# Optimization experiments

Measured on AMD Instinct MI355X. Metric: run time of the kernel, lower is better.

The kernel has to match this reference:

```python
import jax, jax.numpy as jnp
import numpy as np


def lrelu(x):
    return jax.nn.leaky_relu(x, 0.1)


def mask_softmax(a, mask, axis=-1):
    # faithful to the torch version: max over ALL entries, mask applied post-exp
    a_max = jnp.max(a, axis=axis, keepdims=True)
    e = jnp.exp(a - a_max) * mask
    return e / (jnp.sum(e, axis=axis, keepdims=True) + 1e-6)


def gru_cell(x, h, w_ih, w_hh, b_ih, b_hh):
    # torch.nn.GRUCell math; weights stored as [in, 3H]
    gi = x @ w_ih + b_ih
    gh = h @ w_hh + b_hh
    ir, iz, inn = jnp.split(gi, 3, axis=-1)
    hr, hz, hn = jnp.split(gh, 3, axis=-1)
    r = jax.nn.sigmoid(ir + hr)
    z = jax.nn.sigmoid(iz + hz)
    n = jnp.tanh(inn + r * hn)
    return (1 - z) * n + z * h


def setup_inputs() -> dict:
    key = jax.random.key(0)
    B, N, M, E, H, D, K = 128, 256, 12, 256, 128, 3, 2
    AF, BF, NA, NB = 82, 6, 100, 12
    ks = iter(jax.random.split(key, 64))
    nrm = lambda shape: jax.random.normal(next(ks), shape, jnp.float32) * 0.05
    return dict(
        batch_size=B,
        vertex_mask=jnp.ones((B, N), jnp.float32),
        vertex=jax.random.randint(next(ks), (B, N), 0, NA, dtype=jnp.int32),
        edge=jax.random.randint(next(ks), (B, E), 0, NB, dtype=jnp.int32),
        atom_adj=jax.random.randint(next(ks), (B * N * M,), 0, B * N, dtype=jnp.int32),
        bond_adj=jax.random.randint(next(ks), (B * N * M,), 0, B * E, dtype=jnp.int32),
        nbs_mask=jnp.ones((B, N, M), jnp.float32),
        init_atom_features=nrm((NA, AF)),
        init_bond_features=nrm((NB, BF)),
        emb_w=nrm((AF, H)), emb_b=nrm((H,)),
        Wa_main_w=nrm((D, K, H, H)), Wa_main_b=nrm((D, K, H)),
        Wbmm_w=nrm((D, K, H)), Wbmm_b=nrm((D, K)),
        Wmain_w=nrm((D, K, H, H)), Wmain_b=nrm((D, K, H)),
        Wm2s_w=nrm((D, K * H, H)), Wm2s_b=nrm((D, H)),
        Ws2m_w=nrm((D, H, H)), Ws2m_b=nrm((D, H)),
        Wsuper_w=nrm((D, H, H)), Wsuper_b=nrm((D, H)),
        Wzm1_w=nrm((D, H, H)), Wzm1_b=nrm((D, H)),
        Wzm2_w=nrm((D, H, H)), Wzm2_b=nrm((D, H)),
        Wzs1_w=nrm((D, H, H)), Wzs1_b=nrm((D, H)),
        Wzs2_w=nrm((D, H, H)), Wzs2_b=nrm((D, H)),
        U2_w=nrm((D, H + BF, H)), U2_b=nrm((D, H)),
        U1_w=nrm((D, 2 * H, H)), U1_b=nrm((D, H)),
        gm_wih=nrm((H, 3 * H)), gm_whh=nrm((H, 3 * H)), gm_bih=nrm((3 * H,)), gm_bhh=nrm((3 * H,)),
        gs_wih=nrm((H, 3 * H)), gs_whh=nrm((H, 3 * H)), gs_bih=nrm((3 * H,)), gs_bhh=nrm((3 * H,)),
    )


def reference(batch_size, vertex_mask, vertex, edge, atom_adj, bond_adj, nbs_mask,
              init_atom_features, init_bond_features, emb_w, emb_b,
              Wa_main_w, Wa_main_b, Wbmm_w, Wbmm_b, Wmain_w, Wmain_b,
              Wm2s_w, Wm2s_b, Ws2m_w, Ws2m_b, Wsuper_w, Wsuper_b,
              Wzm1_w, Wzm1_b, Wzm2_w, Wzm2_b, Wzs1_w, Wzs1_b, Wzs2_w, Wzs2_b,
              U2_w, U2_b, U1_w, U1_b,
              gm_wih, gm_whh, gm_bih, gm_bhh, gs_wih, gs_whh, gs_bih, gs_bhh):
    B = batch_size
    N = vertex_mask.shape[1]
    M = nbs_mask.shape[2]
    H = emb_w.shape[1]
    BF = init_bond_features.shape[1]
    D, K = Wa_main_w.shape[0], Wa_main_w.shape[1]

    vertex_initial = init_atom_features[vertex]          # [B,N,AF]
    edge_initial = init_bond_features[edge]              # [B,E,BF]
    vf = lrelu(vertex_initial @ emb_w + emb_b)           # [B,N,H]
    vm = vertex_mask[:, :, None]
    sf = jnp.sum(vf * vm, axis=1, keepdims=True)         # [B,1,H] super node

    for d in range(D):
        # multi-head super-node attention (all k heads vectorized)
        a_main = jnp.tanh(jnp.einsum('bnh,khg->bkng', vf, Wa_main_w[d]) + Wa_main_b[d][None, :, None, :])
        a = jnp.einsum('bkng,kg->bkn', a_main * sf[:, None, :, :], Wbmm_w[d]) + Wbmm_b[d][None, :, None]
        attn = mask_softmax(a, vertex_mask[:, None, :])                  # [B,K,N]
        wv = jnp.einsum('bnh,khg->bkng', vf, Wmain_w[d]) + Wmain_b[d][None, :, None, :]
        m = jnp.einsum('bkn,bkng->bkg', attn, wv).reshape(B, 1, K * H)   # head-concat
        main_to_super = jnp.tanh(m @ Wm2s_w[d] + Wm2s_b[d])              # [B,1,H]

        # WLN unit: gather neighbor atom/bond features, fused MLP + masked sum
        vnei = vf.reshape(-1, H)[atom_adj].reshape(B, N, M, H)
        enei = edge_initial.reshape(-1, BF)[bond_adj].reshape(B, N, M, BF)
        nei = jnp.concatenate([vnei, enei], axis=-1)                     # [B,N,M,H+BF]
        nei_label = lrelu(nei @ U2_w[d] + U2_b[d])
        nei_label = jnp.sum(nei_label * nbs_mask[..., None], axis=-2)    # [B,N,H]
        main_self = lrelu(jnp.concatenate([vf, nei_label], axis=-1) @ U1_w[d] + U1_b[d])

        super_to_main = jnp.tanh(sf @ Ws2m_w[d] + Ws2m_b[d])
        super_self = jnp.tanh(sf @ Wsuper_w[d] + Wsuper_b[d])

        z_main = jax.nn.sigmoid(main_self @ Wzm1_w[d] + Wzm1_b[d]
                                + super_to_main @ Wzm2_w[d] + Wzm2_b[d])
        hidden_main = (1 - z_main) * main_self + z_main * super_to_main
        vf = gru_cell(hidden_main.reshape(-1, H), vf.reshape(-1, H),
                      gm_wih, gm_whh, gm_bih, gm_bhh).reshape(B, N, H)

        z_super = jax.nn.sigmoid(super_self @ Wzs1_w[d] + Wzs1_b[d]
                                 + main_to_super @ Wzs2_w[d] + Wzs2_b[d])
        hidden_super = (1 - z_super) * super_self + z_super * main_to_super
        sf = gru_cell(hidden_super.reshape(B, H), sf.reshape(B, H),
                      gs_wih, gs_whh, gs_bih, gs_bhh).reshape(B, 1, H)

    return (vf, sf)
```

## Files before the change

### kernel.cpp

```cpp
#include <hip/hip_runtime.h>

typedef unsigned short ushort_t;
typedef unsigned int uint_t;
typedef unsigned char uchar_t;
typedef __attribute__((ext_vector_type(8))) short short8;
typedef __attribute__((ext_vector_type(4))) float f32x4;
typedef __attribute__((ext_vector_type(2))) float f32x2;

#define B   128
#define Nv  256
#define Mn  12
#define Hd  128
#define Dd  3
#define Kk  2
#define AFd 82
#define BFd 6
#define BN  (B*Nv)

enum { EPI_NONE = 0, EPI_LRELU = 1 };

__device__ __forceinline__ float lrelu(float x) { return fmaxf(x, 0.1f * x); }
__device__ __forceinline__ float sigmoidf(float x) { return 1.f / (1.f + expf(-x)); }
__device__ __forceinline__ ushort_t f2b(float x) {
    uint_t u = __float_as_uint(x);
// ... 230 lines not shown
            for (int nf = 0; nf < 4; ++nf) {
                const int c = wn * 64 + nf * 16 + lr;
                #pragma unroll
                for (int reg = 0; reg < 4; ++reg) {
                    const int r = wm * 32 + mf * 16 + lg * 4 + reg;
                    Pout[(size_t)(row0 + r) * Hd + c] = f2e8(acc[mf][nf][reg] + u2B[c]);
                }
            }
    } else {
        #pragma unroll
        for (int mf = 0; mf < 2; ++mf) {
            #pragma unroll
            for (int reg = 0; reg < 4; ++reg) {
                float p = 0.f;
                #pragma unroll
                for (int nf = 0; nf < 4; ++nf) {
                    const int c = wn * 64 + nf * 16 + lr;
                    p += tanhf(acc[mf][nf][reg] + EBb[c]) * EUs[c];
                }
                p += __shfl_xor(p, 1); p += __shfl_xor(p, 2);
                p += __shfl_xor(p, 4); p += __shfl_xor(p, 8);
                if (lr == 0) red[wm * 32 + mf * 16 + lg * 4 + reg][wn] = p;
            }
        }
        __syncthreads();
        if (t < 64) {
            const int gr = row0 + t;
            a_out[(size_t)(gr >> 8) * 512 + (size_t)ky * 256 + (gr & 255)] =
                red[t][0] + red[t][1] + wbmmB[ky];
        }
    }
}

__global__ __launch_bounds__(256, 3) void k_mega(
    const ushort_t* __restrict__ vfb,
    const uchar_t* __restrict__ P8,
    const ushort_t* __restrict__ qt,
    const int* __restrict__ aadj, const int* __restrict__ badj,
    const int* __restrict__ edge, const float* __restrict__ nmask,
    const ushort_t* __restrict__ wt_u1,
    const ushort_t* __restrict__ wt_zm1,
    const ushort_t* __restrict__ wt_rz,
    const ushort_t* __restrict__ wt_inn,
    const ushort_t* __restrict__ wt_hn,
    const float* __restrict__ u1b,
    const float* __restrict__ zm1b,
    const float* __restrict__ bih, const float* __restrict__ bhh,
    const float* __restrict__ czm2, const float* __restrict__ s2m,
    void* __restrict__ outv, const int finalFp32)
{
    const int t = threadIdx.x;
    const int lane = t & 63, w = t >> 6;
    const int wm = w >> 1, wn = w & 1;
    const int lr = lane & 15, lg = lane >> 4;
    const int row0 = blockIdx.x * 64;
    const int b = row0 >> 8;

    __shared__ ushort_t As[64 * 256];
    __shared__ ushort_t aiS[64 * Mn];
    __shared__ ushort_t eiS[64 * Mn];
    __shared__ ushort_t mkS[64 * Mn];

    for (int i = t; i < 64 * Mn; i += 256) {
        const int r = i / Mn, m = i - r * Mn;
        const long g = (long)(row0 + r) * Mn + m;
        aiS[i] = (ushort_t)aadj[g];
        eiS[i] = (ushort_t)edge[badj[g]];
        mkS[i] = f2b(nmask[g]);
    }
    {
        const int r_st = t >> 2, q4 = t & 3;
        const ushort_t* src = vfb + (size_t)(row0 + r_st) * Hd + q4 * 32;
        #pragma unroll
        for (int j = 0; j < 4; ++j) {
            uint4 v = ((const uint4*)src)[j];
            int byte = r_st * 512 + q4 * 64 + j * 16;
            byte ^= ((r_st & 7) << 4);
            *(uint4*)((char*)As + byte) = v;
        }
    }
    __syncthreads();

    #pragma unroll 1
    for (int it = 0; it < 4; ++it) {
        const int idx = it * 256 + t;
        const int r = idx >> 4, h0 = (idx & 15) * 8;
        float a8[8] = {0.f,0.f,0.f,0.f,0.f,0.f,0.f,0.f};
        #pragma unroll
        for (int m = 0; m < Mn; ++m) {
            const int ai = aiS[r * Mn + m];
            const float mk = b2f(mkS[r * Mn + m]);
            const uint2 pv = *(const uint2*)&P8[(size_t)ai * Hd + h0];
            const uint4 qv = *(const uint4*)&qt[(size_t)eiS[r * Mn + m] * Hd + h0];
            const f32x2 p01 = __builtin_amdgcn_cvt_pk_f32_fp8((int)pv.x, false);
            const f32x2 p23 = __builtin_amdgcn_cvt_pk_f32_fp8((int)pv.x, true);
            const f32x2 p45 = __builtin_amdgcn_cvt_pk_f32_fp8((int)pv.y, false);
            const f32x2 p67 = __builtin_amdgcn_cvt_pk_f32_fp8((int)pv.y, true);
            const float pf[8] = {p01[0], p01[1], p23[0], p23[1], p45[0], p45[1], p67[0], p67[1]};
            const ushort_t* qq = (const ushort_t*)&qv;
            #pragma unroll
            for (int e = 0; e < 8; ++e) {
                const float v = pf[e] + b2f(qq[e]);
                a8[e] = fmaf(mk, lrelu(v), a8[e]);
            }
        }
        ushort_t o8[8];
        #pragma unroll
        for (int e = 0; e < 8; ++e) o8[e] = f2b(a8[e]);
        int byte = r * 512 + (128 + h0) * 2;
        byte ^= ((r & 7) << 4);
        *(uint4*)((char*)As + byte) = *(const uint4*)o8;
    }
    __syncthreads();

    f32x4 acc[2][4];

#define ZERO_ACC() { _Pragma("unroll") for (int i = 0; i < 2; ++i) _Pragma("unroll") for (int j = 0; j < 4; ++j) acc[i][j] = (f32x4){0.f,0.f,0.f,0.f}; }
#define GEMM_PASS(WG, KPADW, KTOT, AOFF_EXPR) { \
        ZERO_ACC(); \
        _Pragma("unroll") \
        for (int kk = 0; kk < (KTOT); kk += 32) { \
            const int acol = (AOFF_EXPR); \
            short8 af[2], bfr[4]; \
            _Pragma("unroll") \
            for (int nf = 0; nf < 4; ++nf) { \
                const int col = wn * 64 + nf * 16 + lr; \
                bfr[nf] = *(const short8*)((WG) + (size_t)col * (KPADW) + kk + lg * 8); \
            } \
            _Pragma("unroll") \
            for (int mf = 0; mf < 2; ++mf) { \
                const int row = wm * 32 + mf * 16 + lr; \
                int byte = row * 512 + (acol + lg * 8) * 2; \
                byte ^= ((row & 7) << 4); \
                af[mf] = *(const short8*)((const char*)As + byte); \
            } \
            _Pragma("unroll") \
            for (int mf = 0; mf < 2; ++mf) \
                _Pragma("unroll") \
                for (int nf = 0; nf < 4; ++nf) \
                    acc[mf][nf] = __builtin_amdgcn_mfma_f32_16x16x32_bf16(af[mf], bfr[nf], acc[mf][nf], 0, 0, 0); \
        } }

    GEMM_PASS(wt_u1, 256, 256, kk);
    {
// ... 91 lines not shown
            const float r2 = sigmoidf(acc[mf][nf][2] + bb);
            const float r3 = sigmoidf(acc[mf][nf][3] + bb);
            const float n0 = tanhf(upk_lo(innp[mf][nf][0]) + r0 * upk_lo(hnp[mf][nf][0]));
            const float n1 = tanhf(upk_hi(innp[mf][nf][0]) + r1 * upk_hi(hnp[mf][nf][0]));
            const float n2 = tanhf(upk_lo(innp[mf][nf][1]) + r2 * upk_lo(hnp[mf][nf][1]));
            const float n3 = tanhf(upk_hi(innp[mf][nf][1]) + r3 * upk_hi(hnp[mf][nf][1]));
            innp[mf][nf][0] = pk2(n0, n1);
            innp[mf][nf][1] = pk2(n2, n3);
        }
    GEMM_PASS(wt_rz + 128 * 256, 256, 256, (kk < 128) ? (128 + kk) : (kk - 128));
    #pragma unroll
    for (int mf = 0; mf < 2; ++mf)
        #pragma unroll
        for (int nf = 0; nf < 4; ++nf) {
            const int c = wn * 64 + nf * 16 + lr;
            const float bb = bih[128 + c] + bhh[128 + c];
            #pragma unroll
            for (int reg = 0; reg < 4; ++reg) {
                const int rl = wm * 32 + mf * 16 + lg * 4 + reg;
                const float z = sigmoidf(acc[mf][nf][reg] + bb);
                const uint_t np = innp[mf][nf][reg >> 1];
                const float n = (reg & 1) ? upk_hi(np) : upk_lo(np);
                int byte = rl * 512 + c * 2;
                byte ^= ((rl & 7) << 4);
                const float h = b2f(*(const ushort_t*)((const char*)As + byte));
                const float o = (1.f - z) * n + z * h;
                const size_t oidx = (size_t)(row0 + rl) * Hd + c;
                if (finalFp32) ((float*)outv)[oidx] = o;
                else           ((ushort_t*)outv)[oidx] = f2b(o);
            }
        }
#undef GEMM_PASS
#undef ZERO_ACC
}

__device__ __forceinline__ void gemv1(const float* __restrict__ W0, const float* __restrict__ x0,
                                      int ldw, int off, int K,
                                      float (*red)[8][32][4],
                                      float* __restrict__ y0, int t)
{
    const int gq = t & 31, hs = t >> 5;
    const int hn = K >> 3;
    f32x4 a0 = (f32x4){0.f,0.f,0.f,0.f};
    const float* Wp0 = W0 + off + (size_t)gq * 4;
    const int h0 = hs * hn;
    #pragma unroll 8
    for (int i = 0; i < hn; ++i) {
        const float4 w0 = *(const float4*)&Wp0[(size_t)(h0 + i) * ldw];
        const float v0 = x0[h0 + i];
        a0.x = fmaf(v0, w0.x, a0.x); a0.y = fmaf(v0, w0.y, a0.y);
        a0.z = fmaf(v0, w0.z, a0.z); a0.w = fmaf(v0, w0.w, a0.w);
    }
    *(f32x4*)&red[0][hs][gq][0] = a0;
    __syncthreads();
    if (t < 128) {
        float s0 = 0.f;
        #pragma unroll
        for (int p = 0; p < 8; ++p) s0 += red[0][p][t >> 2][t & 3];
        y0[t] = s0;
    }
    __syncthreads();
}

__device__ __forceinline__ void gemv2(const float* __restrict__ W0, const float* __restrict__ x0,
                                      const float* __restrict__ W1, const float* __restrict__ x1,
                                      int ldw, int off, int K,
                                      float (*red)[8][32][4],
                                      float* __restrict__ y0, float* __restrict__ y1, int t)
{
    const int gq = t & 31, hs = t >> 5;
    const int hn = K >> 3;
    f32x4 a0 = (f32x4){0.f,0.f,0.f,0.f}, a1 = (f32x4){0.f,0.f,0.f,0.f};
    const float* Wp0 = W0 + off + (size_t)gq * 4;
    const float* Wp1 = W1 + off + (size_t)gq * 4;
    const int h0 = hs * hn;
    #pragma unroll 4
    for (int i = 0; i < hn; ++i) {
        const float4 w0 = *(const float4*)&Wp0[(size_t)(h0 + i) * ldw];
        const float4 w1 = *(const float4*)&Wp1[(size_t)(h0 + i) * ldw];
        const float v0 = x0[h0 + i], v1 = x1[h0 + i];
        a0.x = fmaf(v0, w0.x, a0.x); a0.y = fmaf(v0, w0.y, a0.y);
        a0.z = fmaf(v0, w0.z, a0.z); a0.w = fmaf(v0, w0.w, a0.w);
        a1.x = fmaf(v1, w1.x, a1.x); a1.y = fmaf(v1, w1.y, a1.y);
        a1.z = fmaf(v1, w1.z, a1.z); a1.w = fmaf(v1, w1.w, a1.w);
    }
    *(f32x4*)&red[0][hs][gq][0] = a0;
    *(f32x4*)&red[1][hs][gq][0] = a1;
    __syncthreads();
    if (t < 128) {
        float s0 = 0.f, s1 = 0.f;
        #pragma unroll
        for (int p = 0; p < 8; ++p) {
            s0 += red[0][p][t >> 2][t & 3];
            s1 += red[1][p][t >> 2][t & 3];
        }
        y0[t] = s0; y1[t] = s1;
    }
    __syncthreads();
}

__device__ __forceinline__ void gemv3(const float* __restrict__ W0, const float* __restrict__ x0,
                                      const float* __restrict__ W1, const float* __restrict__ x1,
                                      const float* __restrict__ W2, const float* __restrict__ x2,
                                      int ldw, int off, int K,
                                      float (*red)[8][32][4],
                                      float* __restrict__ y0, float* __restrict__ y1,
                                      float* __restrict__ y2, int t)
{
    const int gq = t & 31, hs = t >> 5;
    const int hn = K >> 3;
    f32x4 a0 = (f32x4){0.f,0.f,0.f,0.f}, a1 = (f32x4){0.f,0.f,0.f,0.f}, a2 = (f32x4){0.f,0.f,0.f,0.f};
    const float* Wp0 = W0 + off + (size_t)gq * 4;
    const float* Wp1 = W1 + off + (size_t)gq * 4;
    const float* Wp2 = W2 + off + (size_t)gq * 4;
    const int h0 = hs * hn;
    #pragma unroll 4
    for (int i = 0; i < hn; ++i) {
        const float4 w0 = *(const float4*)&Wp0[(size_t)(h0 + i) * ldw];
        const float4 w1 = *(const float4*)&Wp1[(size_t)(h0 + i) * ldw];
        const float4 w2 = *(const float4*)&Wp2[(size_t)(h0 + i) * ldw];
        const float v0 = x0[h0 + i], v1 = x1[h0 + i], v2 = x2[h0 + i];
        a0.x = fmaf(v0, w0.x, a0.x); a0.y = fmaf(v0, w0.y, a0.y);
        a0.z = fmaf(v0, w0.z, a0.z); a0.w = fmaf(v0, w0.w, a0.w);
        a1.x = fmaf(v1, w1.x, a1.x); a1.y = fmaf(v1, w1.y, a1.y);
        a1.z = fmaf(v1, w1.z, a1.z); a1.w = fmaf(v1, w1.w, a1.w);
        a2.x = fmaf(v2, w2.x, a2.x); a2.y = fmaf(v2, w2.y, a2.y);
        a2.z = fmaf(v2, w2.z, a2.z); a2.w = fmaf(v2, w2.w, a2.w);
    }
    *(f32x4*)&red[0][hs][gq][0] = a0;
    *(f32x4*)&red[1][hs][gq][0] = a1;
    *(f32x4*)&red[2][hs][gq][0] = a2;
    __syncthreads();
    if (t < 128) {
        float s0 = 0.f, s1 = 0.f, s2 = 0.f;
        #pragma unroll
        for (int p = 0; p < 8; ++p) {
            s0 += red[0][p][t >> 2][t & 3];
            s1 += red[1][p][t >> 2][t & 3];
            s2 += red[2][p][t >> 2][t & 3];
        }
        y0[t] = s0; y1[t] = s1; y2[t] = s2;
    }
    __syncthreads();
}

__global__ __launch_bounds__(256) void k_super(
    const float* __restrict__ a_buf, const float* __restrict__ vmask,
    const ushort_t* __restrict__ vfb,
    const float* __restrict__ sf_in,
    const float* __restrict__ Wm, const float* __restrict__ bm,
    const float* __restrict__ Wm2s, const float* __restrict__ bm2s,
    const float* __restrict__ Ws2m, const float* __restrict__ bs2m,
    const float* __restrict__ Wsup, const float* __restrict__ bsup,
    const float* __restrict__ Wzm2, const float* __restrict__ bzm2,
    const float* __restrict__ Wzs1, const float* __restrict__ bzs1,
    const float* __restrict__ Wzs2, const float* __restrict__ bzs2,
    const float* __restrict__ gwih, const float* __restrict__ gwhh,
    const float* __restrict__ gbih, const float* __restrict__ gbhh,
    float* __restrict__ s2m_g, float* __restrict__ czm2_g,
    float* __restrict__ sf_out)
{
    const int b = blockIdx.x, t = threadIdx.x;
    const int wid = t >> 6, lane = t & 63;
    __shared__ float red[3][8][32][4];
    __shared__ float att0[256], att1[256];
    __shared__ float sfl[128], tbA[128], tbB[128], mv[256];
    __shared__ float ms2[128], s2ml[128], ssl[128], hsl[128];
    __shared__ float tmp1[128], tmp2[128], tmp3[128];
    __shared__ float gib[384], ghb[384];
    __shared__ float saS[2];
    __shared__ float lm[4][2], ls[4][2];

    const float v0 = a_buf[(size_t)b * 512 + t];
    const float v1 = a_buf[(size_t)b * 512 + 256 + t];
    const float vm = vmask[b * Nv + t];
    float m0 = v0, m1 = v1;
    #pragma unroll
    for (int o = 1; o < 64; o <<= 1) {
        m0 = fmaxf(m0, __shfl_xor(m0, o));
        m1 = fmaxf(m1, __shfl_xor(m1, o));
    }
    if (lane == 0) { lm[wid][0] = m0; lm[wid][1] = m1; }
    __syncthreads();
    m0 = fmaxf(fmaxf(lm[0][0], lm[1][0]), fmaxf(lm[2][0], lm[3][0]));
    m1 = fmaxf(fmaxf(lm[0][1], lm[1][1]), fmaxf(lm[2][1], lm[3][1]));
    const float e0v = expf(v0 - m0) * vm;
    const float e1v = expf(v1 - m1) * vm;
    float s0 = e0v, s1 = e1v;
    #pragma unroll
    for (int o = 1; o < 64; o <<= 1) {
        s0 += __shfl_xor(s0, o);
        s1 += __shfl_xor(s1, o);
    }
    if (lane == 0) { ls[wid][0] = s0; ls[wid][1] = s1; }
    if (t < 128) sfl[t] = sf_in[b * Hd + t];
    __syncthreads();
    s0 = ls[0][0] + ls[1][0] + ls[2][0] + ls[3][0];
    s1 = ls[0][1] + ls[1][1] + ls[2][1] + ls[3][1];
    att0[t] = e0v / (s0 + 1e-6f);
    att1[t] = e1v / (s1 + 1e-6f);
    if (t == 0) { saS[0] = s0 / (s0 + 1e-6f); saS[1] = s1 / (s1 + 1e-6f); }
    __syncthreads();

    {
        const int hq = t & 31, ns = t >> 5;
        f32x4 a0 = (f32x4){0.f,0.f,0.f,0.f}, a1 = (f32x4){0.f,0.f,0.f,0.f};
        const ushort_t* base = vfb + (size_t)b * Nv * Hd + hq * 4;
        #pragma unroll 8
        for (int i = 0; i < 32; ++i) {
            const int n = ns * 32 + i;
            float xv[4];
            b2f4(*(const uint2*)&base[(size_t)n * Hd], xv);
            const float w0 = att0[n], w1 = att1[n];
            a0.x = fmaf(w0, xv[0], a0.x); a0.y = fmaf(w0, xv[1], a0.y);
            a0.z = fmaf(w0, xv[2], a0.z); a0.w = fmaf(w0, xv[3], a0.w);
            a1.x = fmaf(w1, xv[0], a1.x); a1.y = fmaf(w1, xv[1], a1.y);
            a1.z = fmaf(w1, xv[2], a1.z); a1.w = fmaf(w1, xv[3], a1.w);
        }
        *(f32x4*)&red[0][ns][hq][0] = a0;
        *(f32x4*)&red[1][ns][hq][0] = a1;
        __syncthreads();
        if (t < 128) {
            float u0 = 0.f, u1 = 0.f;
            #pragma unroll
            for (int p = 0; p < 8; ++p) {
                u0 += red[0][p][t >> 2][t & 3];
                u1 += red[1][p][t >> 2][t & 3];
            }
            tbA[t] = u0; tbB[t] = u1;
        }
        __syncthreads();
    }

    gemv2(Wm, tbA, Wm + Hd * Hd, tbB, Hd, 0, Hd, red, mv, mv + 128, t);
    mv[t] += saS[t >> 7] * bm[t];
    __syncthreads();

    gemv1(Wm2s, mv, Hd, 0, 2 * Hd, red, tmp1, t);
    if (t < 128) ms2[t] = tanhf(tmp1[t] + bm2s[t]);
    __syncthreads();

    gemv2(Ws2m, sfl, Wsup, sfl, Hd, 0, Hd, red, tmp1, tmp2, t);
    if (t < 128) {
        const float v = tanhf(tmp1[t] + bs2m[t]);
        s2ml[t] = v; s2m_g[b * Hd + t] = v;
        ssl[t] = tanhf(tmp2[t] + bsup[t]);
    }
    __syncthreads();

    gemv3(Wzm2, s2ml, Wzs1, ssl, Wzs2, ms2, Hd, 0, Hd, red, tmp1, tmp2, tmp3, t);
    if (t < 128) {
        czm2_g[b * Hd + t] = tmp1[t] + bzm2[t];
        const float zs = sigmoidf(tmp2[t] + bzs1[t] + tmp3[t] + bzs2[t]);
        hsl[t] = (1.f - zs) * ssl[t] + zs * ms2[t];
    }
    __syncthreads();

    #pragma unroll 1
    for (int c = 0; c < 3; ++c)
        gemv2(gwih, hsl, gwhh, sfl, 3 * Hd, c * Hd, Hd, red, gib + c * Hd, ghb + c * Hd, t);
    if (t < 128) {
        const float r = sigmoidf(gib[t] + gbih[t] + ghb[t] + gbhh[t]);
        const float z = sigmoidf(gib[128 + t] + gbih[128 + t] + ghb[128 + t] + gbhh[128 + t]);
        const float n = tanhf(gib[256 + t] + gbih[256 + t] + r * (ghb[256 + t] + gbhh[256 + t]));
        sf_out[b * Hd + t] = (1.f - z) * n + z * sfl[t];
    }
}

__global__ __launch_bounds__(256) void k_sfv(const ushort_t* __restrict__ vfb,
                                             const float* __restrict__ vmask,
                                             float* __restrict__ sf)
{
    const int b = blockIdx.x, t = threadIdx.x;
    __shared__ float vm[256];
    __shared__ float red[8][32][4];
    vm[t] = vmask[b * Nv + t];
    __syncthreads();
    const int hq = t & 31, ns = t >> 5;
    f32x4 acc = (f32x4){0.f,0.f,0.f,0.f};
    const ushort_t* base = vfb + (size_t)b * Nv * Hd + hq * 4;
    #pragma unroll 8
    for (int i = 0; i < 32; ++i) {
        const int n = ns * 32 + i;
        float xv[4];
        b2f4(*(const uint2*)&base[(size_t)n * Hd], xv);
        const float w = vm[n];
        acc.x = fmaf(w, xv[0], acc.x); acc.y = fmaf(w, xv[1], acc.y);
        acc.z = fmaf(w, xv[2], acc.z); acc.w = fmaf(w, xv[3], acc.w);
    }
    *(f32x4*)&red[ns][hq][0] = acc;
    __syncthreads();
    if (t < 128) {
        float s = 0.f;
        #pragma unroll
        for (int p = 0; p < 8; ++p) s += red[p][t >> 2][t & 3];
        sf[b * Hd + t] = s;
    }
}

// ... 23 lines not shown
    const float* Wm2s_b = (const float*)d_in[18];
    const float* Ws2m_w = (const float*)d_in[19];
    const float* Ws2m_b = (const float*)d_in[20];
    const float* Wsup_w = (const float*)d_in[21];
    const float* Wsup_b = (const float*)d_in[22];
    const float* Wzm1_w = (const float*)d_in[23];
    const float* Wzm1_b = (const float*)d_in[24];
    const float* Wzm2_w = (const float*)d_in[25];
    const float* Wzm2_b = (const float*)d_in[26];
    const float* Wzs1_w = (const float*)d_in[27];
    const float* Wzs1_b = (const float*)d_in[28];
    const float* Wzs2_w = (const float*)d_in[29];
    const float* Wzs2_b = (const float*)d_in[30];
    const float* U2_w   = (const float*)d_in[31];
    const float* U2_b   = (const float*)d_in[32];
    const float* U1_w   = (const float*)d_in[33];
    const float* U1_b   = (const float*)d_in[34];
    const float* gm_wih = (const float*)d_in[35];
    const float* gm_whh = (const float*)d_in[36];
    const float* gm_bih = (const float*)d_in[37];
    const float* gm_bhh = (const float*)d_in[38];
    const float* gs_wih = (const float*)d_in[39];
    const float* gs_whh = (const float*)d_in[40];
    const float* gs_bih = (const float*)d_in[41];
    const float* gs_bhh = (const float*)d_in[42];

    const size_t MB = 1u << 20;
    if (ws_size < 40 * MB) return;

    char* base = (char*)d_ws;
    ushort_t* VF0 = (ushort_t*)base;
    ushort_t* VF1 = (ushort_t*)(base + 8 * MB);
    uchar_t*  P8  = (uchar_t*)(base + 16 * MB);
    ushort_t* WT  = (ushort_t*)(base + 24 * MB);
    ushort_t* QT  = (ushort_t*)(base + 26 * MB);
    float*    S   = (float*)(base + 27 * MB);

    float* sfA    = S;
    float* sfB    = S + 16384;
    float* a_buf  = S + 32768;
    float* s2m    = S + 98304;
    float* c_zm2  = S + 114688;

    float* X1 = (float*)d_out;
    float* sf_final = X1 + (size_t)BN * Hd;

    const int OFF_EMB = 0;
    const int PERD = 98304;
    const int OFF_L0 = 16384;
    const int OFF_RZ = OFF_L0 + 3 * PERD;
    const int OFF_NH = OFF_RZ + 65536;

    PrepJobs PJ;
    int nj = 0, blk0 = 0;
    auto addJob = [&](const float* W, int K, int ldw, long sStride, int nPer,
                      int Kspan, int KpadRow, int kDst, int ncols, int outOff) {
        PrepJob& J = PJ.j[nj++];
        J.W = W; J.K = K; J.ldw = ldw; J.sliceStride = sStride; J.nPerSlice = nPer;
        J.Kspan = Kspan; J.KpadRow = KpadRow; J.kDst = kDst;
        J.total = ncols * Kspan; J.outOff = outOff; J.blockStart = blk0;
        blk0 += (J.total + 255) / 256;
    };
    addJob(emb_w, AFd, Hd, 0, Hd, 128, 128, 0, 128, OFF_EMB);
    for (int d = 0; d < Dd; ++d) {
        const int o = OFF_L0 + d * PERD;
        addJob(Wa_w + (long)d * Kk * Hd * Hd, Hd, Hd, (long)Hd * Hd, Hd, 128, 128, 0, 256, o);
        addJob(U2_w + (long)d * (Hd + BFd) * Hd, Hd, Hd, 0, Hd, 128, 128, 0, 128, o + 32768);
        addJob(U1_w + (long)d * 2 * Hd * Hd, 2 * Hd, Hd, 0, Hd, 256, 256, 0, 128, o + 49152);
        addJob(Wzm1_w + (long)d * Hd * Hd, Hd, Hd, 0, Hd, 128, 128, 0, 128, o + 81920);
    }
    addJob(gm_wih, Hd, 3 * Hd, 0, 256, 128, 256, 0,   256, OFF_RZ);
    addJob(gm_whh, Hd, 3 * Hd, 0, 256, 128, 256, 128, 256, OFF_RZ);
    addJob(gm_wih + 256, Hd, 3 * Hd, 0, 128, 128, 128, 0, 128, OFF_NH);
    addJob(gm_whh + 256, Hd, 3 * Hd, 0, 128, 128, 128, 0, 128, OFF_NH + 16384);
    PJ.nJobs = nj;
    k_prep_all<<<dim3(blk0), dim3(256), 0, stream>>>(PJ, WT);
    k_qtab<<<dim3(Dd), dim3(256), 0, stream>>>(init_bond, U2_w, QT);

    const dim3 blk(256);
    const dim3 g1(BN / 64, 1);

    mgemm<EPI_LRELU, false, true><<<g1, blk, 0, stream>>>(
        init_atom, AFd, AFd, vertex,
        WT + OFF_EMB, 128, emb_b, VF0, Hd);
    k_sfv<<<dim3(B), blk, 0, stream>>>(VF0, vertex_mask, sfA);

    for (int d = 0; d < Dd; ++d) {
        ushort_t* vin  = (d & 1) ? VF1 : VF0;
        ushort_t* vout = (d & 1) ? VF0 : VF1;
        float* sin  = (d & 1) ? sfB : sfA;
        float* sout = (d == Dd - 1) ? sf_final : ((d & 1) ? sfA : sfB);

        const int o = OFF_L0 + d * PERD;

        k_tdp<<<dim3(BN / 64, 3), blk, 0, stream>>>(
            vin, WT + o,
            Wa_b + (long)d * Kk * Hd, U2_b + (long)d * Hd,
            sin, Wbmm_w + (long)d * Kk * Hd, Wbmm_b + (long)d * Kk,
            a_buf, P8);

        k_super<<<dim3(B), blk, 0, stream>>>(
            a_buf, vertex_mask, vin, sin,
            Wm_w + (long)d * Kk * Hd * Hd, Wm_b + (long)d * Kk * Hd,
            Wm2s_w + (long)d * Kk * Hd * Hd, Wm2s_b + (long)d * Hd,
            Ws2m_w + (long)d * Hd * Hd, Ws2m_b + (long)d * Hd,
            Wsup_w + (long)d * Hd * Hd, Wsup_b + (long)d * Hd,
            Wzm2_w + (long)d * Hd * Hd, Wzm2_b + (long)d * Hd,
            Wzs1_w + (long)d * Hd * Hd, Wzs1_b + (long)d * Hd,
            Wzs2_w + (long)d * Hd * Hd, Wzs2_b + (long)d * Hd,
            gs_wih, gs_whh, gs_bih, gs_bhh,
            s2m, c_zm2, sout);

        k_mega<<<g1, blk, 0, stream>>>(
            vin, P8, QT + (size_t)d * 12 * Hd,
            atom_adj, bond_adj, edge, nbs_mask,
            WT + o + 49152, WT + o + 81920,
            WT + OFF_RZ, WT + OFF_NH, WT + OFF_NH + 16384,
            U1_b + (long)d * Hd, Wzm1_b + (long)d * Hd,
            gm_bih, gm_bhh,
            c_zm2, s2m,
            (d == Dd - 1) ? (void*)X1 : (void*)vout, (d == Dd - 1) ? 1 : 0);
    }
}
```

Measured before the change: 343.4 us.

## Move neighbor gather into super-node kernel to overlap with serial GEMV work

The per-atom neighbor gather-and-reduce (fp8 P plus bond Q, leaky-relu, masked sum) moves out of k_mega into extra blocks of the super-node kernel, which writes the result to a new NEI workspace buffer. k_super ran only 128 blocks of serial GEMVs, so the gather blocks can fill the idle CUs alongside them, and k_mega now just loads the precomputed NEI rows into shared memory. The cost is an extra global write and read of a 64K×128 bf16 buffer, plus a larger combined launch whose blocks differ in shared-memory footprint.

```diff
diff --git a/kernel.cpp b/kernel.cpp
--- a/kernel.cpp
+++ b/kernel.cpp
@@ -286,12 +286,292 @@
     }
 }
 
+__device__ __forceinline__ void gemv1(const float* __restrict__ W0, const float* __restrict__ x0,
+                                      int ldw, int off, int K,
+                                      float (*red)[8][32][4],
+                                      float* __restrict__ y0, int t)
+{
+    const int gq = t & 31, hs = t >> 5;
+    const int hn = K >> 3;
+    f32x4 a0 = (f32x4){0.f,0.f,0.f,0.f};
+    const float* Wp0 = W0 + off + (size_t)gq * 4;
+    const int h0 = hs * hn;
+    #pragma unroll 8
+    for (int i = 0; i < hn; ++i) {
+        const float4 w0 = *(const float4*)&Wp0[(size_t)(h0 + i) * ldw];
+        const float v0 = x0[h0 + i];
+        a0.x = fmaf(v0, w0.x, a0.x); a0.y = fmaf(v0, w0.y, a0.y);
+        a0.z = fmaf(v0, w0.z, a0.z); a0.w = fmaf(v0, w0.w, a0.w);
+    }
+    *(f32x4*)&red[0][hs][gq][0] = a0;
+    __syncthreads();
+    if (t < 128) {
+        float s0 = 0.f;
+        #pragma unroll
+        for (int p = 0; p < 8; ++p) s0 += red[0][p][t >> 2][t & 3];
+        y0[t] = s0;
+    }
+    __syncthreads();
+}
+
+__device__ __forceinline__ void gemv2(const float* __restrict__ W0, const float* __restrict__ x0,
+                                      const float* __restrict__ W1, const float* __restrict__ x1,
+                                      int ldw, int off, int K,
+                                      float (*red)[8][32][4],
+                                      float* __restrict__ y0, float* __restrict__ y1, int t)
+{
+    const int gq = t & 31, hs = t >> 5;
+    const int hn = K >> 3;
+    f32x4 a0 = (f32x4){0.f,0.f,0.f,0.f}, a1 = (f32x4){0.f,0.f,0.f,0.f};
+    const float* Wp0 = W0 + off + (size_t)gq * 4;
+    const float* Wp1 = W1 + off + (size_t)gq * 4;
+    const int h0 = hs * hn;
+    #pragma unroll 4
+    for (int i = 0; i < hn; ++i) {
+        const float4 w0 = *(const float4*)&Wp0[(size_t)(h0 + i) * ldw];
+        const float4 w1 = *(const float4*)&Wp1[(size_t)(h0 + i) * ldw];
+        const float v0 = x0[h0 + i], v1 = x1[h0 + i];
+        a0.x = fmaf(v0, w0.x, a0.x); a0.y = fmaf(v0, w0.y, a0.y);
+        a0.z = fmaf(v0, w0.z, a0.z); a0.w = fmaf(v0, w0.w, a0.w);
+        a1.x = fmaf(v1, w1.x, a1.x); a1.y = fmaf(v1, w1.y, a1.y);
+        a1.z = fmaf(v1, w1.z, a1.z); a1.w = fmaf(v1, w1.w, a1.w);
+    }
+    *(f32x4*)&red[0][hs][gq][0] = a0;
+    *(f32x4*)&red[1][hs][gq][0] = a1;
+    __syncthreads();
+    if (t < 128) {
+        float s0 = 0.f, s1 = 0.f;
+        #pragma unroll
+        for (int p = 0; p < 8; ++p) {
+            s0 += red[0][p][t >> 2][t & 3];
+            s1 += red[1][p][t >> 2][t & 3];
+        }
+        y0[t] = s0; y1[t] = s1;
+    }
+    __syncthreads();
+}
+
+__device__ __forceinline__ void gemv3(const float* __restrict__ W0, const float* __restrict__ x0,
+                                      const float* __restrict__ W1, const float* __restrict__ x1,
+                                      const float* __restrict__ W2, const float* __restrict__ x2,
+                                      int ldw, int off, int K,
+                                      float (*red)[8][32][4],
+                                      float* __restrict__ y0, float* __restrict__ y1,
+                                      float* __restrict__ y2, int t)
+{
+    const int gq = t & 31, hs = t >> 5;
+    const int hn = K >> 3;
+    f32x4 a0 = (f32x4){0.f,0.f,0.f,0.f}, a1 = (f32x4){0.f,0.f,0.f,0.f}, a2 = (f32x4){0.f,0.f,0.f,0.f};
+    const float* Wp0 = W0 + off + (size_t)gq * 4;
+    const float* Wp1 = W1 + off + (size_t)gq * 4;
+    const float* Wp2 = W2 + off + (size_t)gq * 4;
+    const int h0 = hs * hn;
+    #pragma unroll 4
+    for (int i = 0; i < hn; ++i) {
+        const float4 w0 = *(const float4*)&Wp0[(size_t)(h0 + i) * ldw];
+        const float4 w1 = *(const float4*)&Wp1[(size_t)(h0 + i) * ldw];
+        const float4 w2 = *(const float4*)&Wp2[(size_t)(h0 + i) * ldw];
+        const float v0 = x0[h0 + i], v1 = x1[h0 + i], v2 = x2[h0 + i];
+        a0.x = fmaf(v0, w0.x, a0.x); a0.y = fmaf(v0, w0.y, a0.y);
+        a0.z = fmaf(v0, w0.z, a0.z); a0.w = fmaf(v0, w0.w, a0.w);
+        a1.x = fmaf(v1, w1.x, a1.x); a1.y = fmaf(v1, w1.y, a1.y);
+        a1.z = fmaf(v1, w1.z, a1.z); a1.w = fmaf(v1, w1.w, a1.w);
+        a2.x = fmaf(v2, w2.x, a2.x); a2.y = fmaf(v2, w2.y, a2.y);
+        a2.z = fmaf(v2, w2.z, a2.z); a2.w = fmaf(v2, w2.w, a2.w);
+    }
+    *(f32x4*)&red[0][hs][gq][0] = a0;
+    *(f32x4*)&red[1][hs][gq][0] = a1;
+    *(f32x4*)&red[2][hs][gq][0] = a2;
+    __syncthreads();
+    if (t < 128) {
+        float s0 = 0.f, s1 = 0.f, s2 = 0.f;
+        #pragma unroll
+        for (int p = 0; p < 8; ++p) {
+            s0 += red[0][p][t >> 2][t & 3];
+            s1 += red[1][p][t >> 2][t & 3];
+            s2 += red[2][p][t >> 2][t & 3];
+        }
+        y0[t] = s0; y1[t] = s1; y2[t] = s2;
+    }
+    __syncthreads();
+}
+
+__global__ __launch_bounds__(256) void k_gsup(
+    const float* __restrict__ a_buf, const float* __restrict__ vmask,
+    const ushort_t* __restrict__ vfb,
+    const float* __restrict__ sf_in,
+    const float* __restrict__ Wm, const float* __restrict__ bm,
+    const float* __restrict__ Wm2s, const float* __restrict__ bm2s,
+    const float* __restrict__ Ws2m, const float* __restrict__ bs2m,
+    const float* __restrict__ Wsup, const float* __restrict__ bsup,
+    const float* __restrict__ Wzm2, const float* __restrict__ bzm2,
+    const float* __restrict__ Wzs1, const float* __restrict__ bzs1,
+    const float* __restrict__ Wzs2, const float* __restrict__ bzs2,
+    const float* __restrict__ gwih, const float* __restrict__ gwhh,
+    const float* __restrict__ gbih, const float* __restrict__ gbhh,
+    float* __restrict__ s2m_g, float* __restrict__ czm2_g,
+    float* __restrict__ sf_out,
+    const uchar_t* __restrict__ P8, const ushort_t* __restrict__ qt,
+    const int* __restrict__ aadj, const int* __restrict__ badj,
+    const int* __restrict__ edge, const float* __restrict__ nmask,
+    ushort_t* __restrict__ nei)
+{
+    const int t = threadIdx.x;
+
+    if (blockIdx.x >= B) {
+        __shared__ ushort_t aiS[64 * Mn];
+        __shared__ ushort_t eiS[64 * Mn];
+        __shared__ ushort_t mkS[64 * Mn];
+        const int row0 = (blockIdx.x - B) * 64;
+        for (int i = t; i < 64 * Mn; i += 256) {
+            const int r = i / Mn, m = i - r * Mn;
+            const long g = (long)(row0 + r) * Mn + m;
+            aiS[i] = (ushort_t)aadj[g];
+            eiS[i] = (ushort_t)edge[badj[g]];
+            mkS[i] = f2b(nmask[g]);
+        }
+        __syncthreads();
+        #pragma unroll 1
+        for (int it = 0; it < 4; ++it) {
+            const int idx = it * 256 + t;
+            const int r = idx >> 4, h0 = (idx & 15) * 8;
+            float a8[8] = {0.f,0.f,0.f,0.f,0.f,0.f,0.f,0.f};
+            #pragma unroll
+            for (int m = 0; m < Mn; ++m) {
+                const int ai = aiS[r * Mn + m];
+                const float mk = b2f(mkS[r * Mn + m]);
+                const uint2 pv = *(const uint2*)&P8[(size_t)ai * Hd + h0];
+                const uint4 qv = *(const uint4*)&qt[(size_t)eiS[r * Mn + m] * Hd + h0];
+                const f32x2 p01 = __builtin_amdgcn_cvt_pk_f32_fp8((int)pv.x, false);
+                const f32x2 p23 = __builtin_amdgcn_cvt_pk_f32_fp8((int)pv.x, true);
+                const f32x2 p45 = __builtin_amdgcn_cvt_pk_f32_fp8((int)pv.y, false);
+                const f32x2 p67 = __builtin_amdgcn_cvt_pk_f32_fp8((int)pv.y, true);
+                const float pf[8] = {p01[0], p01[1], p23[0], p23[1], p45[0], p45[1], p67[0], p67[1]};
+                const ushort_t* qq = (const ushort_t*)&qv;
+                #pragma unroll
+                for (int e = 0; e < 8; ++e) {
+                    const float v = pf[e] + b2f(qq[e]);
+                    a8[e] = fmaf(mk, lrelu(v), a8[e]);
+                }
+            }
+            ushort_t o8[8];
+            #pragma unroll
+            for (int e = 0; e < 8; ++e) o8[e] = f2b(a8[e]);
+            *(uint4*)&nei[(size_t)(row0 + r) * Hd + h0] = *(const uint4*)o8;
+        }
+        return;
+    }
+
+    const int b = blockIdx.x;
+    const int wid = t >> 6, lane = t & 63;
+    __shared__ float red[3][8][32][4];
+    __shared__ float att0[256], att1[256];
+    __shared__ float sfl[128], tbA[128], tbB[128], mv[256];
+    __shared__ float ms2[128], s2ml[128], ssl[128], hsl[128];
+    __shared__ float tmp1[128], tmp2[128], tmp3[128];
+    __shared__ float gib[384], ghb[384];
+    __shared__ float saS[2];
+    __shared__ float lm[4][2], ls[4][2];
+
+    const float v0 = a_buf[(size_t)b * 512 + t];
+    const float v1 = a_buf[(size_t)b * 512 + 256 + t];
+    const float vm = vmask[b * Nv + t];
+    float m0 = v0, m1 = v1;
+    #pragma unroll
+    for (int o = 1; o < 64; o <<= 1) {
+        m0 = fmaxf(m0, __shfl_xor(m0, o));
+        m1 = fmaxf(m1, __shfl_xor(m1, o));
+    }
+    if (lane == 0) { lm[wid][0] = m0; lm[wid][1] = m1; }
+    __syncthreads();
+    m0 = fmaxf(fmaxf(lm[0][0], lm[1][0]), fmaxf(lm[2][0], lm[3][0]));
+    m1 = fmaxf(fmaxf(lm[0][1], lm[1][1]), fmaxf(lm[2][1], lm[3][1]));
+    const float e0v = expf(v0 - m0) * vm;
+    const float e1v = expf(v1 - m1) * vm;
+    float s0 = e0v, s1 = e1v;
+    #pragma unroll
+    for (int o = 1; o < 64; o <<= 1) {
+        s0 += __shfl_xor(s0, o);
+        s1 += __shfl_xor(s1, o);
+    }
+    if (lane == 0) { ls[wid][0] = s0; ls[wid][1] = s1; }
+    if (t < 128) sfl[t] = sf_in[b * Hd + t];
+    __syncthreads();
+    s0 = ls[0][0] + ls[1][0] + ls[2][0] + ls[3][0];
+    s1 = ls[0][1] + ls[1][1] + ls[2][1] + ls[3][1];
+    att0[t] = e0v / (s0 + 1e-6f);
+    att1[t] = e1v / (s1 + 1e-6f);
+    if (t == 0) { saS[0] = s0 / (s0 + 1e-6f); saS[1] = s1 / (s1 + 1e-6f); }
+    __syncthreads();
+
+    {
+        const int hq = t & 31, ns = t >> 5;
+        f32x4 a0 = (f32x4){0.f,0.f,0.f,0.f}, a1 = (f32x4){0.f,0.f,0.f,0.f};
+        const ushort_t* base = vfb + (size_t)b * Nv * Hd + hq * 4;
+        #pragma unroll 8
+        for (int i = 0; i < 32; ++i) {
+            const int n = ns * 32 + i;
+            float xv[4];
+            b2f4(*(const uint2*)&base[(size_t)n * Hd], xv);
+            const float w0 = att0[n], w1 = att1[n];
+            a0.x = fmaf(w0, xv[0], a0.x); a0.y = fmaf(w0, xv[1], a0.y);
+            a0.z = fmaf(w0, xv[2], a0.z); a0.w = fmaf(w0, xv[3], a0.w);
+            a1.x = fmaf(w1, xv[0], a1.x); a1.y = fmaf(w1, xv[1], a1.y);
+            a1.z = fmaf(w1, xv[2], a1.z); a1.w = fmaf(w1, xv[3], a1.w);
+        }
+        *(f32x4*)&red[0][ns][hq][0] = a0;
+        *(f32x4*)&red[1][ns][hq][0] = a1;
+        __syncthreads();
+        if (t < 128) {
+            float u0 = 0.f, u1 = 0.f;
+            #pragma unroll
+            for (int p = 0; p < 8; ++p) {
+                u0 += red[0][p][t >> 2][t & 3];
+                u1 += red[1][p][t >> 2][t & 3];
+            }
+            tbA[t] = u0; tbB[t] = u1;
+        }
+        __syncthreads();
+    }
+
+    gemv2(Wm, tbA, Wm + Hd * Hd, tbB, Hd, 0, Hd, red, mv, mv + 128, t);
+    mv[t] += saS[t >> 7] * bm[t];
+    __syncthreads();
+
+    gemv1(Wm2s, mv, Hd, 0, 2 * Hd, red, tmp1, t);
+    if (t < 128) ms2[t] = tanhf(tmp1[t] + bm2s[t]);
+    __syncthreads();
+
+    gemv2(Ws2m, sfl, Wsup, sfl, Hd, 0, Hd, red, tmp1, tmp2, t);
+    if (t < 128) {
+        const float v = tanhf(tmp1[t] + bs2m[t]);
+        s2ml[t] = v; s2m_g[b * Hd + t] = v;
+        ssl[t] = tanhf(tmp2[t] + bsup[t]);
+    }
+    __syncthreads();
+
+    gemv3(Wzm2, s2ml, Wzs1, ssl, Wzs2, ms2, Hd, 0, Hd, red, tmp1, tmp2, tmp3, t);
+    if (t < 128) {
+        czm2_g[b * Hd + t] = tmp1[t] + bzm2[t];
+        const float zs = sigmoidf(tmp2[t] + bzs1[t] + tmp3[t] + bzs2[t]);
+        hsl[t] = (1.f - zs) * ssl[t] + zs * ms2[t];
+    }
+    __syncthreads();
+
+    #pragma unroll 1
+    for (int c = 0; c < 3; ++c)
+        gemv2(gwih, hsl, gwhh, sfl, 3 * Hd, c * Hd, Hd, red, gib + c * Hd, ghb + c * Hd, t);
+    if (t < 128) {
+        const float r = sigmoidf(gib[t] + gbih[t] + ghb[t] + gbhh[t]);
+        const float z = sigmoidf(gib[128 + t] + gbih[128 + t] + ghb[128 + t] + gbhh[128 + t]);
+        const float n = tanhf(gib[256 + t] + gbih[256 + t] + r * (ghb[256 + t] + gbhh[256 + t]));
+        sf_out[b * Hd + t] = (1.f - z) * n + z * sfl[t];
+    }
+}
+
 __global__ __launch_bounds__(256, 3) void k_mega(
     const ushort_t* __restrict__ vfb,
-    const uchar_t* __restrict__ P8,
-    const ushort_t* __restrict__ qt,
-    const int* __restrict__ aadj, const int* __restrict__ badj,
-    const int* __restrict__ edge, const float* __restrict__ nmask,
+    const ushort_t* __restrict__ nei,
     const ushort_t* __restrict__ wt_u1,
     const ushort_t* __restrict__ wt_zm1,
     const ushort_t* __restrict__ wt_rz,
@@ -311,59 +591,23 @@
     const int b = row0 >> 8;
 
     __shared__ ushort_t As[64 * 256];
-    __shared__ ushort_t aiS[64 * Mn];
-    __shared__ ushort_t eiS[64 * Mn];
-    __shared__ ushort_t mkS[64 * Mn];
-
-    for (int i = t; i < 64 * Mn; i += 256) {
-        const int r = i / Mn, m = i - r * Mn;
-        const long g = (long)(row0 + r) * Mn + m;
-        aiS[i] = (ushort_t)aadj[g];
-        eiS[i] = (ushort_t)edge[badj[g]];
-        mkS[i] = f2b(nmask[g]);
-    }
+
     {
         const int r_st = t >> 2, q4 = t & 3;
-        const ushort_t* src = vfb + (size_t)(row0 + r_st) * Hd + q4 * 32;
+        const ushort_t* srcV = vfb + (size_t)(row0 + r_st) * Hd + q4 * 32;
+        const ushort_t* srcN = nei + (size_t)(row0 + r_st) * Hd + q4 * 32;
         #pragma unroll
         for (int j = 0; j < 4; ++j) {
-            uint4 v = ((const uint4*)src)[j];
-            int byte = r_st * 512 + q4 * 64 + j * 16;
-            byte ^= ((r_st & 7) << 4);
+            uint4 v = ((const uint4*)srcV)[j];
+            int byte = (r_st * 512 + q4 * 64 + j * 16) ^ ((r_st & 7) << 4);
             *(uint4*)((char*)As + byte) = v;
         }
-    }
-    __syncthreads();
-
-    #pragma unroll 1
-    for (int it = 0; it < 4; ++it) {
-        const int idx = it * 256 + t;
-        const int r = idx >> 4, h0 = (idx & 15) * 8;
-        float a8[8] = {0.f,0.f,0.f,0.f,0.f,0.f,0.f,0.f};
-        #pragma unroll
-        for (int m = 0; m < Mn; ++m) {
-            const int ai = aiS[r * Mn + m];
-            const float mk = b2f(mkS[r * Mn + m]);
-            const uint2 pv = *(const uint2*)&P8[(size_t)ai * Hd + h0];
-            const uint4 qv = *(const uint4*)&qt[(size_t)eiS[r * Mn + m] * Hd + h0];
-            const f32x2 p01 = __builtin_amdgcn_cvt_pk_f32_fp8((int)pv.x, false);
-            const f32x2 p23 = __builtin_amdgcn_cvt_pk_f32_fp8((int)pv.x, true);
-            const f32x2 p45 = __builtin_amdgcn_cvt_pk_f32_fp8((int)pv.y, false);
-            const f32x2 p67 = __builtin_amdgcn_cvt_pk_f32_fp8((int)pv.y, true);
-            const float pf[8] = {p01[0], p01[1], p23[0], p23[1], p45[0], p45[1], p67[0], p67[1]};
-            const ushort_t* qq = (const ushort_t*)&qv;
-            #pragma unroll
-            for (int e = 0; e < 8; ++e) {
-                const float v = pf[e] + b2f(qq[e]);
-                a8[e] = fmaf(mk, lrelu(v), a8[e]);
-            }
-        }
-        ushort_t o8[8];
-        #pragma unroll
-        for (int e = 0; e < 8; ++e) o8[e] = f2b(a8[e]);
-        int byte = r * 512 + (128 + h0) * 2;
-        byte ^= ((r & 7) << 4);
-        *(uint4*)((char*)As + byte) = *(const uint4*)o8;
+        #pragma unroll
+        for (int j = 0; j < 4; ++j) {
+            uint4 v = ((const uint4*)srcN)[j];
+            int byte = (r_st * 512 + 256 + q4 * 64 + j * 16) ^ ((r_st & 7) << 4);
+            *(uint4*)((char*)As + byte) = v;
+        }
     }
     __syncthreads();
 
@@ -521,239 +765,6 @@
         }
 #undef GEMM_PASS
 #undef ZERO_ACC
-}
-
-__device__ __forceinline__ void gemv1(const float* __restrict__ W0, const float* __restrict__ x0,
-                                      int ldw, int off, int K,
-                                      float (*red)[8][32][4],
-                                      float* __restrict__ y0, int t)
-{
-    const int gq = t & 31, hs = t >> 5;
-    const int hn = K >> 3;
-    f32x4 a0 = (f32x4){0.f,0.f,0.f,0.f};
-    const float* Wp0 = W0 + off + (size_t)gq * 4;
-    const int h0 = hs * hn;
-    #pragma unroll 8
-    for (int i = 0; i < hn; ++i) {
-        const float4 w0 = *(const float4*)&Wp0[(size_t)(h0 + i) * ldw];
-        const float v0 = x0[h0 + i];
-        a0.x = fmaf(v0, w0.x, a0.x); a0.y = fmaf(v0, w0.y, a0.y);
-        a0.z = fmaf(v0, w0.z, a0.z); a0.w = fmaf(v0, w0.w, a0.w);
-    }
-    *(f32x4*)&red[0][hs][gq][0] = a0;
-    __syncthreads();
-    if (t < 128) {
-        float s0 = 0.f;
-        #pragma unroll
-        for (int p = 0; p < 8; ++p) s0 += red[0][p][t >> 2][t & 3];
-        y0[t] = s0;
-    }
-    __syncthreads();
-}
-
-__device__ __forceinline__ void gemv2(const float* __restrict__ W0, const float* __restrict__ x0,
-                                      const float* __restrict__ W1, const float* __restrict__ x1,
-                                      int ldw, int off, int K,
-                                      float (*red)[8][32][4],
-                                      float* __restrict__ y0, float* __restrict__ y1, int t)
-{
-    const int gq = t & 31, hs = t >> 5;
-    const int hn = K >> 3;
-    f32x4 a0 = (f32x4){0.f,0.f,0.f,0.f}, a1 = (f32x4){0.f,0.f,0.f,0.f};
-    const float* Wp0 = W0 + off + (size_t)gq * 4;
-    const float* Wp1 = W1 + off + (size_t)gq * 4;
-    const int h0 = hs * hn;
-    #pragma unroll 4
-    for (int i = 0; i < hn; ++i) {
-        const float4 w0 = *(const float4*)&Wp0[(size_t)(h0 + i) * ldw];
-        const float4 w1 = *(const float4*)&Wp1[(size_t)(h0 + i) * ldw];
-        const float v0 = x0[h0 + i], v1 = x1[h0 + i];
-        a0.x = fmaf(v0, w0.x, a0.x); a0.y = fmaf(v0, w0.y, a0.y);
-        a0.z = fmaf(v0, w0.z, a0.z); a0.w = fmaf(v0, w0.w, a0.w);
-        a1.x = fmaf(v1, w1.x, a1.x); a1.y = fmaf(v1, w1.y, a1.y);
-        a1.z = fmaf(v1, w1.z, a1.z); a1.w = fmaf(v1, w1.w, a1.w);
-    }
-    *(f32x4*)&red[0][hs][gq][0] = a0;
-    *(f32x4*)&red[1][hs][gq][0] = a1;
-    __syncthreads();
-    if (t < 128) {
-        float s0 = 0.f, s1 = 0.f;
-        #pragma unroll
-        for (int p = 0; p < 8; ++p) {
-            s0 += red[0][p][t >> 2][t & 3];
-            s1 += red[1][p][t >> 2][t & 3];
-        }
-        y0[t] = s0; y1[t] = s1;
-    }
-    __syncthreads();
-}
-
-__device__ __forceinline__ void gemv3(const float* __restrict__ W0, const float* __restrict__ x0,
-                                      const float* __restrict__ W1, const float* __restrict__ x1,
-                                      const float* __restrict__ W2, const float* __restrict__ x2,
-                                      int ldw, int off, int K,
-                                      float (*red)[8][32][4],
-                                      float* __restrict__ y0, float* __restrict__ y1,
-                                      float* __restrict__ y2, int t)
-{
-    const int gq = t & 31, hs = t >> 5;
-    const int hn = K >> 3;
-    f32x4 a0 = (f32x4){0.f,0.f,0.f,0.f}, a1 = (f32x4){0.f,0.f,0.f,0.f}, a2 = (f32x4){0.f,0.f,0.f,0.f};
-    const float* Wp0 = W0 + off + (size_t)gq * 4;
-    const float* Wp1 = W1 + off + (size_t)gq * 4;
-    const float* Wp2 = W2 + off + (size_t)gq * 4;
-    const int h0 = hs * hn;
-    #pragma unroll 4
-    for (int i = 0; i < hn; ++i) {
-        const float4 w0 = *(const float4*)&Wp0[(size_t)(h0 + i) * ldw];
-        const float4 w1 = *(const float4*)&Wp1[(size_t)(h0 + i) * ldw];
-        const float4 w2 = *(const float4*)&Wp2[(size_t)(h0 + i) * ldw];
-        const float v0 = x0[h0 + i], v1 = x1[h0 + i], v2 = x2[h0 + i];
-        a0.x = fmaf(v0, w0.x, a0.x); a0.y = fmaf(v0, w0.y, a0.y);
-        a0.z = fmaf(v0, w0.z, a0.z); a0.w = fmaf(v0, w0.w, a0.w);
-        a1.x = fmaf(v1, w1.x, a1.x); a1.y = fmaf(v1, w1.y, a1.y);
-        a1.z = fmaf(v1, w1.z, a1.z); a1.w = fmaf(v1, w1.w, a1.w);
-        a2.x = fmaf(v2, w2.x, a2.x); a2.y = fmaf(v2, w2.y, a2.y);
-        a2.z = fmaf(v2, w2.z, a2.z); a2.w = fmaf(v2, w2.w, a2.w);
-    }
-    *(f32x4*)&red[0][hs][gq][0] = a0;
-    *(f32x4*)&red[1][hs][gq][0] = a1;
-    *(f32x4*)&red[2][hs][gq][0] = a2;
-    __syncthreads();
-    if (t < 128) {
-        float s0 = 0.f, s1 = 0.f, s2 = 0.f;
-        #pragma unroll
-        for (int p = 0; p < 8; ++p) {
-            s0 += red[0][p][t >> 2][t & 3];
-            s1 += red[1][p][t >> 2][t & 3];
-            s2 += red[2][p][t >> 2][t & 3];
-        }
-        y0[t] = s0; y1[t] = s1; y2[t] = s2;
-    }
-    __syncthreads();
-}
-
-__global__ __launch_bounds__(256) void k_super(
-    const float* __restrict__ a_buf, const float* __restrict__ vmask,
-    const ushort_t* __restrict__ vfb,
-    const float* __restrict__ sf_in,
-    const float* __restrict__ Wm, const float* __restrict__ bm,
-    const float* __restrict__ Wm2s, const float* __restrict__ bm2s,
-    const float* __restrict__ Ws2m, const float* __restrict__ bs2m,
-    const float* __restrict__ Wsup, const float* __restrict__ bsup,
-    const float* __restrict__ Wzm2, const float* __restrict__ bzm2,
-    const float* __restrict__ Wzs1, const float* __restrict__ bzs1,
-    const float* __restrict__ Wzs2, const float* __restrict__ bzs2,
-    const float* __restrict__ gwih, const float* __restrict__ gwhh,
-    const float* __restrict__ gbih, const float* __restrict__ gbhh,
-    float* __restrict__ s2m_g, float* __restrict__ czm2_g,
-    float* __restrict__ sf_out)
-{
-    const int b = blockIdx.x, t = threadIdx.x;
-    const int wid = t >> 6, lane = t & 63;
-    __shared__ float red[3][8][32][4];
-    __shared__ float att0[256], att1[256];
-    __shared__ float sfl[128], tbA[128], tbB[128], mv[256];
-    __shared__ float ms2[128], s2ml[128], ssl[128], hsl[128];
-    __shared__ float tmp1[128], tmp2[128], tmp3[128];
-    __shared__ float gib[384], ghb[384];
-    __shared__ float saS[2];
-    __shared__ float lm[4][2], ls[4][2];
-
-    const float v0 = a_buf[(size_t)b * 512 + t];
-    const float v1 = a_buf[(size_t)b * 512 + 256 + t];
-    const float vm = vmask[b * Nv + t];
-    float m0 = v0, m1 = v1;
-    #pragma unroll
-    for (int o = 1; o < 64; o <<= 1) {
-        m0 = fmaxf(m0, __shfl_xor(m0, o));
-        m1 = fmaxf(m1, __shfl_xor(m1, o));
-    }
-    if (lane == 0) { lm[wid][0] = m0; lm[wid][1] = m1; }
-    __syncthreads();
-    m0 = fmaxf(fmaxf(lm[0][0], lm[1][0]), fmaxf(lm[2][0], lm[3][0]));
-    m1 = fmaxf(fmaxf(lm[0][1], lm[1][1]), fmaxf(lm[2][1], lm[3][1]));
-    const float e0v = expf(v0 - m0) * vm;
-    const float e1v = expf(v1 - m1) * vm;
-    float s0 = e0v, s1 = e1v;
-    #pragma unroll
-    for (int o = 1; o < 64; o <<= 1) {
-        s0 += __shfl_xor(s0, o);
-        s1 += __shfl_xor(s1, o);
-    }
-    if (lane == 0) { ls[wid][0] = s0; ls[wid][1] = s1; }
-    if (t < 128) sfl[t] = sf_in[b * Hd + t];
-    __syncthreads();
-    s0 = ls[0][0] + ls[1][0] + ls[2][0] + ls[3][0];
-    s1 = ls[0][1] + ls[1][1] + ls[2][1] + ls[3][1];
-    att0[t] = e0v / (s0 + 1e-6f);
-    att1[t] = e1v / (s1 + 1e-6f);
-    if (t == 0) { saS[0] = s0 / (s0 + 1e-6f); saS[1] = s1 / (s1 + 1e-6f); }
-    __syncthreads();
-
-    {
-        const int hq = t & 31, ns = t >> 5;
-        f32x4 a0 = (f32x4){0.f,0.f,0.f,0.f}, a1 = (f32x4){0.f,0.f,0.f,0.f};
-        const ushort_t* base = vfb + (size_t)b * Nv * Hd + hq * 4;
-        #pragma unroll 8
-        for (int i = 0; i < 32; ++i) {
-            const int n = ns * 32 + i;
-            float xv[4];
-            b2f4(*(const uint2*)&base[(size_t)n * Hd], xv);
-            const float w0 = att0[n], w1 = att1[n];
-            a0.x = fmaf(w0, xv[0], a0.x); a0.y = fmaf(w0, xv[1], a0.y);
-            a0.z = fmaf(w0, xv[2], a0.z); a0.w = fmaf(w0, xv[3], a0.w);
-            a1.x = fmaf(w1, xv[0], a1.x); a1.y = fmaf(w1, xv[1], a1.y);
-            a1.z = fmaf(w1, xv[2], a1.z); a1.w = fmaf(w1, xv[3], a1.w);
-        }
-        *(f32x4*)&red[0][ns][hq][0] = a0;
-        *(f32x4*)&red[1][ns][hq][0] = a1;
-        __syncthreads();
-        if (t < 128) {
-            float u0 = 0.f, u1 = 0.f;
-            #pragma unroll
-            for (int p = 0; p < 8; ++p) {
-                u0 += red[0][p][t >> 2][t & 3];
-                u1 += red[1][p][t >> 2][t & 3];
-            }
-            tbA[t] = u0; tbB[t] = u1;
-        }
-        __syncthreads();
-    }
-
-    gemv2(Wm, tbA, Wm + Hd * Hd, tbB, Hd, 0, Hd, red, mv, mv + 128, t);
-    mv[t] += saS[t >> 7] * bm[t];
-    __syncthreads();
-
-    gemv1(Wm2s, mv, Hd, 0, 2 * Hd, red, tmp1, t);
-    if (t < 128) ms2[t] = tanhf(tmp1[t] + bm2s[t]);
-    __syncthreads();
-
-    gemv2(Ws2m, sfl, Wsup, sfl, Hd, 0, Hd, red, tmp1, tmp2, t);
-    if (t < 128) {
-        const float v = tanhf(tmp1[t] + bs2m[t]);
-        s2ml[t] = v; s2m_g[b * Hd + t] = v;
-        ssl[t] = tanhf(tmp2[t] + bsup[t]);
-    }
-    __syncthreads();
-
-    gemv3(Wzm2, s2ml, Wzs1, ssl, Wzs2, ms2, Hd, 0, Hd, red, tmp1, tmp2, tmp3, t);
-    if (t < 128) {
-        czm2_g[b * Hd + t] = tmp1[t] + bzm2[t];
-        const float zs = sigmoidf(tmp2[t] + bzs1[t] + tmp3[t] + bzs2[t]);
-        hsl[t] = (1.f - zs) * ssl[t] + zs * ms2[t];
-    }
-    __syncthreads();
-
-    #pragma unroll 1
-    for (int c = 0; c < 3; ++c)
-        gemv2(gwih, hsl, gwhh, sfl, 3 * Hd, c * Hd, Hd, red, gib + c * Hd, ghb + c * Hd, t);
-    if (t < 128) {
-        const float r = sigmoidf(gib[t] + gbih[t] + ghb[t] + gbhh[t]);
-        const float z = sigmoidf(gib[128 + t] + gbih[128 + t] + ghb[128 + t] + gbhh[128 + t]);
-        const float n = tanhf(gib[256 + t] + gbih[256 + t] + r * (ghb[256 + t] + gbhh[256 + t]));
-        sf_out[b * Hd + t] = (1.f - z) * n + z * sfl[t];
-    }
 }
 
 __global__ __launch_bounds__(256) void k_sfv(const ushort_t* __restrict__ vfb,
@@ -843,9 +854,10 @@
     ushort_t* VF0 = (ushort_t*)base;
     ushort_t* VF1 = (ushort_t*)(base + 8 * MB);
     uchar_t*  P8  = (uchar_t*)(base + 16 * MB);
-    ushort_t* WT  = (ushort_t*)(base + 24 * MB);
-    ushort_t* QT  = (ushort_t*)(base + 26 * MB);
-    float*    S   = (float*)(base + 27 * MB);
+    ushort_t* NEI = (ushort_t*)(base + 20 * MB);
+    ushort_t* WT  = (ushort_t*)(base + 28 * MB);
+    ushort_t* QT  = (ushort_t*)(base + 30 * MB);
+    float*    S   = (float*)(base + 31 * MB);
 
     float* sfA    = S;
     float* sfB    = S + 16384;
@@ -910,7 +922,7 @@
             sin, Wbmm_w + (long)d * Kk * Hd, Wbmm_b + (long)d * Kk,
             a_buf, P8);
 
-        k_super<<<dim3(B), blk, 0, stream>>>(
+        k_gsup<<<dim3(B + BN / 64), blk, 0, stream>>>(
             a_buf, vertex_mask, vin, sin,
             Wm_w + (long)d * Kk * Hd * Hd, Wm_b + (long)d * Kk * Hd,
             Wm2s_w + (long)d * Kk * Hd * Hd, Wm2s_b + (long)d * Hd,
@@ -920,11 +932,12 @@
             Wzs1_w + (long)d * Hd * Hd, Wzs1_b + (long)d * Hd,
             Wzs2_w + (long)d * Hd * Hd, Wzs2_b + (long)d * Hd,
             gs_wih, gs_whh, gs_bih, gs_bhh,
-            s2m, c_zm2, sout);
+            s2m, c_zm2, sout,
+            P8, QT + (size_t)d * 12 * Hd,
+            atom_adj, bond_adj, edge, nbs_mask, NEI);
 
         k_mega<<<g1, blk, 0, stream>>>(
-            vin, P8, QT + (size_t)d * 12 * Hd,
-            atom_adj, bond_adj, edge, nbs_mask,
+            vin, NEI,
             WT + o + 49152, WT + o + 81920,
             WT + OFF_RZ, WT + OFF_NH, WT + OFF_NH + 16384,
             U1_b + (long)d * Hd, Wzm1_b + (long)d * Hd,
```

Result: faster. 333.3 us (-2.9%).
